# Optimization experiments

Hardware: AMD Instinct MI355X
Metric: run time of the kernel (lower is better)

## Reference

```python
import jax, jax.numpy as jnp
import numpy as np

N_NODES = 60000
N_EDGES = 240000
N_REL = 4
N_GRAPHS = 128
D_IN = 768
D_H = 256
N_LAYERS = 6


def setup_inputs() -> dict:
    key = jax.random.key(0)
    ks = jax.random.split(key, 16)
    x = jax.random.normal(ks[0], (N_NODES, D_IN), dtype=jnp.float32)
    edge_index = jax.random.randint(ks[1], (2, N_EDGES), 0, N_NODES, dtype=jnp.int64)
    edge_attr = jax.random.randint(ks[2], (N_EDGES,), 0, N_REL, dtype=jnp.int64)
    batch = jnp.sort(jax.random.randint(ks[3], (N_NODES,), 0, N_GRAPHS, dtype=jnp.int64))
    s0 = 1.0 / np.sqrt(D_IN)
    s1 = 1.0 / np.sqrt(D_H)
    w0 = jax.random.normal(ks[4], (N_REL, D_IN, D_H), dtype=jnp.float32) * s0
    root0 = jax.random.normal(ks[5], (D_IN, D_H), dtype=jnp.float32) * s0
    b0 = jnp.zeros((D_H,), jnp.float32)
    w_rest = jax.random.normal(ks[6], (N_LAYERS - 1, N_REL, D_H, D_H), dtype=jnp.float32) * s1
    root_rest = jax.random.normal(ks[7], (N_LAYERS - 1, D_H, D_H), dtype=jnp.float32) * s1
    b_rest = jnp.zeros((N_LAYERS - 1, D_H), jnp.float32)
    fc1_w = jax.random.normal(ks[8], (2 * D_H, 128), dtype=jnp.float32) * (1.0 / np.sqrt(2 * D_H))
    fc1_b = jnp.zeros((128,), jnp.float32)
    fc2_w = jax.random.normal(ks[9], (128, 1), dtype=jnp.float32) * (1.0 / np.sqrt(128))
    fc2_b = jnp.zeros((1,), jnp.float32)
    return {"x": x, "edge_index": edge_index, "edge_attr": edge_attr, "batch": batch,
            "w0": w0, "root0": root0, "b0": b0,
            "w_rest": w_rest, "root_rest": root_rest, "b_rest": b_rest,
            "fc1_w": fc1_w, "fc1_b": fc1_b, "fc2_w": fc2_w, "fc2_b": fc2_b}


def _rgcn(h, src, dst, rel, W, root, b):
    # PyG RGCNConv with aggr='mean': per-relation mean over incoming edges,
    # transformed by per-relation weight, plus root transform and bias.
    n = h.shape[0]
    seg = rel * n + dst                                   # combined (relation, target) segment id
    msgs = h[src]                                         # [E, d_in] gather
    agg = jax.ops.segment_sum(msgs, seg, num_segments=N_REL * n)
    agg = agg.reshape(N_REL, n, -1)                       # [R, N, d_in]
    cnt = jax.ops.segment_sum(jnp.ones_like(rel, jnp.float32), seg, num_segments=N_REL * n)
    cnt = cnt.reshape(N_REL, n, 1)
    mean = agg / jnp.maximum(cnt, 1.0)                    # mean aggregation; 0 for isolated nodes
    return jnp.einsum('rnd,rdo->no', mean, W) + h @ root + b


def reference(x, edge_index, edge_attr, batch, w0, root0, b0,
              w_rest, root_rest, b_rest, fc1_w, fc1_b, fc2_w, fc2_b):
    src, dst = edge_index[0], edge_index[1]
    h = jax.nn.relu(_rgcn(x, src, dst, edge_attr, w0, root0, b0))
    for i in range(N_LAYERS - 1):
        h = jax.nn.relu(_rgcn(h, src, dst, edge_attr, w_rest[i], root_rest[i], b_rest[i]))
    # global mean / max pooling over graphs
    sums = jax.ops.segment_sum(h, batch, num_segments=N_GRAPHS)
    cnt = jax.ops.segment_sum(jnp.ones((h.shape[0],), jnp.float32), batch, num_segments=N_GRAPHS)[:, None]
    h_mean = sums / jnp.maximum(cnt, 1.0)
    h_max = jax.ops.segment_max(h, batch, num_segments=N_GRAPHS)
    h_max = jnp.where(cnt > 0, h_max, 0.0)
    g = jnp.concatenate([h_mean, h_max], axis=1)          # [G, 512]
    out = jax.nn.relu(g @ fc1_w + fc1_b)                  # dropout is identity at inference
    out = out @ fc2_w + fc2_b
    return jax.nn.sigmoid(out.squeeze(-1))                # [G]
```

## Files before the change

kernel.cpp:

```cpp
#include <hip/hip_runtime.h>
#include <hip/hip_bf16.h>

#define N_NODES  60000
#define N_EDGES  240000
#define N_REL    4
#define N_GRAPHS 128
#define D_IN     768
#define D_H      256
#define N_LAYERS 6
#define M_PAD    60032
#define N_TOT    1280
#define BM_L     64
#define LDM      264

static inline int cdiv(int a, int b) { return (a + b - 1) / b; }

typedef __attribute__((ext_vector_type(8))) short short8;
typedef __attribute__((ext_vector_type(4))) float f32x4;

__device__ __forceinline__ float bf2f(unsigned short u) {
    union { unsigned int i; float f; } c; c.i = ((unsigned int)u) << 16; return c.f;
}
__device__ __forceinline__ float bflo(unsigned int u) {
    union { unsigned int i; float f; } c; c.i = u << 16; return c.f;
}
__device__ __forceinline__ float bfhi(unsigned int u) {
    union { unsigned int i; float f; } c; c.i = u & 0xffff0000u; return c.f;
}
__device__ __forceinline__ unsigned short f2bf(float f) {
    union { float f; unsigned int i; } c; c.f = f;
    unsigned int i = c.i;
    unsigned int r = (i + 0x7FFFu + ((i >> 16) & 1u)) >> 16;
    return (unsigned short)r;
}

__device__ __forceinline__ void gload16(const void* g, void* l) {
    __builtin_amdgcn_global_load_lds((const __attribute__((address_space(1))) void*)g,
                                     (__attribute__((address_space(3))) void*)l, 16, 0, 0);
}

__device__ __forceinline__ void accum32(float4* am, uint4 v0, uint4 v1, uint4 v2, uint4 v3) {
    am[0].x += bflo(v0.x); am[0].y += bfhi(v0.x);
    am[0].z += bflo(v0.y); am[0].w += bfhi(v0.y);
    am[1].x += bflo(v0.z); am[1].y += bfhi(v0.z);
    am[1].z += bflo(v0.w); am[1].w += bfhi(v0.w);
    am[2].x += bflo(v1.x); am[2].y += bfhi(v1.x);
    am[2].z += bflo(v1.y); am[2].w += bfhi(v1.y);
    am[3].x += bflo(v1.z); am[3].y += bfhi(v1.z);
    am[3].z += bflo(v1.w); am[3].w += bfhi(v1.w);
    am[4].x += bflo(v2.x); am[4].y += bfhi(v2.x);
    am[4].z += bflo(v2.y); am[4].w += bfhi(v2.y);
    am[5].x += bflo(v2.z); am[5].y += bfhi(v2.z);
    am[5].z += bflo(v2.w); am[5].w += bfhi(v2.w);
    am[6].x += bflo(v3.x); am[6].y += bfhi(v3.x);
    am[6].z += bflo(v3.y); am[6].w += bfhi(v3.y);
    am[7].x += bflo(v3.z); am[7].y += bfhi(v3.z);
    am[7].z += bflo(v3.w); am[7].w += bfhi(v3.w);
}

__global__ __launch_bounds__(512) void gemm_l0(
    const unsigned short* __restrict__ A,
    const unsigned short* __restrict__ Bt,
    const float* __restrict__ bias,
    unsigned short* __restrict__ out_root,
    unsigned short* __restrict__ out_msg,
    int K)
{
    __shared__ unsigned short As[128 * 32];
    __shared__ unsigned short Bs[256 * 32];

    const int tid  = threadIdx.x;
    const int wave = tid >> 6, lane = tid & 63;

    int b = blockIdx.x;
    int bm, bn;
    if (b < 2320) { int grp = b / 40, rem = b % 40; bm = (grp * 8 + (rem & 7)) * 128; bn = (rem >> 3) * 256; }
    else          { int rem = b - 2320; bm = (464 + rem % 5) * 128; bn = (rem / 5) * 256; }

    const int wm = (wave & 1) * 64, wn = (wave >> 1) * 64;

    const int lr = lane >> 2;
    const int kg = ((lane & 3) ^ ((lr ^ (lr >> 2)) & 3)) * 8;
    const unsigned short* gsrc[3];
    unsigned short* ldst[3];
    #pragma unroll
    for (int j = 0; j < 3; ++j) {
        int g = wave * 3 + j;
        if (g < 8) {
            gsrc[j] = A + (size_t)(bm + g * 16 + lr) * K + kg;
            ldst[j] = As + g * 16 * 32;
        } else {
            gsrc[j] = Bt + (size_t)(bn + (g - 8) * 16 + lr) * K + kg;
            ldst[j] = Bs + (g - 8) * 16 * 32;
        }
    }

    f32x4 acc[4][4] = {};
    const int fr = lane & 15;
    const int qsw = (((lane >> 4) ^ fr ^ (fr >> 2)) & 3) * 8;

    for (int k0 = 0; k0 < K; k0 += 32) {
        gload16(gsrc[0] + k0, ldst[0]);
        gload16(gsrc[1] + k0, ldst[1]);
        gload16(gsrc[2] + k0, ldst[2]);
        __syncthreads();

        short8 a[4], bb[4];
        #pragma unroll
        for (int t = 0; t < 4; ++t) {
            a[t]  = *(const short8*)&As[(wm + t * 16 + fr) * 32 + qsw];
            bb[t] = *(const short8*)&Bs[(wn + t * 16 + fr) * 32 + qsw];
        }
        #pragma unroll
        for (int mt = 0; mt < 4; ++mt)
            #pragma unroll
            for (int nt = 0; nt < 4; ++nt)
                acc[mt][nt] = __builtin_amdgcn_mfma_f32_16x16x32_bf16(
                    a[mt], bb[nt], acc[mt][nt], 0, 0, 0);
        __syncthreads();
    }

    const bool is_root = (bn == 0);
    #pragma unroll
    for (int mt = 0; mt < 4; ++mt) {
        #pragma unroll
        for (int nt = 0; nt < 4; ++nt) {
            int col = bn + wn + nt * 16 + fr;
            float bv = bias[col];
            #pragma unroll
            for (int r = 0; r < 4; ++r) {
                int row = bm + wm + mt * 16 + ((lane >> 4) << 2) + r;
                float v = acc[mt][nt][r] + bv;
                if (is_root) out_root[(size_t)row * 256 + col] = f2bf(v);
                else         out_msg[(size_t)row * 1024 + (col - 256)] = f2bf(v);
            }
        }
    }
}

__global__ __launch_bounds__(512) void rgcn_layer(
    const unsigned short* __restrict__ h,
    const unsigned short* __restrict__ Wl,
    const float* __restrict__ bias,
    const int* __restrict__ rp4,
    const int* __restrict__ e_srcs,
    const float* __restrict__ inv4,
    unsigned short* __restrict__ h_out)
{
    __shared__ unsigned short mt[BM_L * LDM];

    const int tid  = threadIdx.x;
    const int wave = tid >> 6, lane = tid & 63;
    const int bm = blockIdx.x * BM_L;

    const int node  = bm + lane;
    const int cq    = wave * 32;
    const bool valid = node < N_NODES;

    const int fr   = lane & 15;
    const int q8   = (lane >> 4) * 8;
    const int wcol = wave * 32;

    const unsigned short* w0p = Wl + (size_t)(wcol + fr) * N_TOT + q8;
    const unsigned short* w1p = Wl + (size_t)(wcol + 16 + fr) * N_TOT + q8;

    float4 iv = valid ? *(const float4*)&inv4[(size_t)node * 4]
                      : make_float4(1.f, 1.f, 1.f, 1.f);

    f32x4 acc[4][2] = {};

    for (int r = 0; r < 5; ++r) {
        float4 am[8];
        #pragma unroll
        for (int j = 0; j < 8; ++j) am[j] = make_float4(0.f, 0.f, 0.f, 0.f);

        if (r < 4) {
            if (valid) {
                int lo = rp4[(size_t)node * 4 + r];
                int hi = rp4[(size_t)node * 4 + r + 1];
                int e = lo;
                for (; e + 1 < hi; e += 2) {
                    const uint4* p0 = (const uint4*)(h + (size_t)e_srcs[e] * 256 + cq);
                    const uint4* p1 = (const uint4*)(h + (size_t)e_srcs[e + 1] * 256 + cq);
                    uint4 v0 = p0[0], v1 = p0[1], v2 = p0[2], v3 = p0[3];
                    uint4 u0 = p1[0], u1 = p1[1], u2 = p1[2], u3 = p1[3];
                    accum32(am, v0, v1, v2, v3);
                    accum32(am, u0, u1, u2, u3);
                }
                if (e < hi) {
                    const uint4* p0 = (const uint4*)(h + (size_t)e_srcs[e] * 256 + cq);
                    accum32(am, p0[0], p0[1], p0[2], p0[3]);
                }
            }
        } else {
            const uint4* p0 = (const uint4*)(h + (size_t)node * 256 + cq);
            accum32(am, p0[0], p0[1], p0[2], p0[3]);
        }
        float sc = (r == 0) ? iv.x : (r == 1) ? iv.y : (r == 2) ? iv.z
                 : (r == 3) ? iv.w : 1.f;

        __syncthreads();
        {
            unsigned short* dst = &mt[lane * LDM + cq];
            #pragma unroll
            for (int j = 0; j < 8; ++j) {
                ushort4 o;
                o.x = f2bf(am[j].x * sc); o.y = f2bf(am[j].y * sc);
                o.z = f2bf(am[j].z * sc); o.w = f2bf(am[j].w * sc);
                *(ushort4*)(dst + j * 4) = o;
            }
        }
        __syncthreads();

        const int rOff = (r << 8);
        #pragma unroll
        for (int kk = 0; kk < 8; ++kk) {
            short8 b0 = *(const short8*)(w0p + rOff + kk * 32);
            short8 b1 = *(const short8*)(w1p + rOff + kk * 32);
            short8 a[4];
            #pragma unroll
            for (int i = 0; i < 4; ++i)
                a[i] = *(const short8*)&mt[(i * 16 + fr) * LDM + kk * 32 + q8];
            #pragma unroll
            for (int i = 0; i < 4; ++i) {
                acc[i][0] = __builtin_amdgcn_mfma_f32_16x16x32_bf16(a[i], b0, acc[i][0], 0, 0, 0);
                acc[i][1] = __builtin_amdgcn_mfma_f32_16x16x32_bf16(a[i], b1, acc[i][1], 0, 0, 0);
            }
        }
    }

    #pragma unroll
    for (int i = 0; i < 4; ++i) {
        #pragma unroll
        for (int nt = 0; nt < 2; ++nt) {
            int col = wcol + nt * 16 + fr;
            float bv = bias[col];
            #pragma unroll
            for (int rg = 0; rg < 4; ++rg) {
                int row = bm + i * 16 + ((lane >> 4) << 2) + rg;
                float v = fmaxf(acc[i][nt][rg] + bv, 0.f);
                h_out[(size_t)row * 256 + col] = f2bf(v);
            }
        }
    }
}

__global__ void convert_x(const float* __restrict__ x, unsigned short* __restrict__ xb) {
    size_t i = ((size_t)blockIdx.x * 256 + threadIdx.x) * 4;
    if (i >= (size_t)M_PAD * D_IN) return;
    ushort4 o;
    if (i < (size_t)N_NODES * D_IN) {
        float4 v = *(const float4*)&x[i];
        o.x = f2bf(v.x); o.y = f2bf(v.y); o.z = f2bf(v.z); o.w = f2bf(v.w);
    } else {
        o.x = o.y = o.z = o.w = 0;
    }
    *(ushort4*)&xb[i] = o;
}

__global__ void pack_w0(const float* __restrict__ root0, const float* __restrict__ w0,
                        unsigned short* __restrict__ Wt0) {
    int idx = blockIdx.x * 256 + threadIdx.x;
    if (idx >= N_TOT * D_IN) return;
    int k = idx % D_IN, n = idx / D_IN;
    float v = (n < 256) ? root0[k * 256 + n]
                        : w0[(((n >> 8) - 1) * D_IN + k) * 256 + (n & 255)];
    Wt0[idx] = f2bf(v);
}

__global__ void pack_wr(const float* __restrict__ root_rest, const float* __restrict__ w_rest,
                        unsigned short* __restrict__ WtR) {
    int idx = blockIdx.x * 256 + threadIdx.x;
    if (idx >= 5 * 256 * N_TOT) return;
    int k = idx % N_TOT; int t = idx / N_TOT; int n = t & 255; int l = t >> 8;
    float v = (k < 1024)
        ? w_rest[(((l * 4 + (k >> 8)) * 256) + (k & 255)) * 256 + n]
        : root_rest[(l * 256 + (k - 1024)) * 256 + n];
    WtR[idx] = f2bf(v);
}

__global__ void build_bias(const float* __restrict__ b0, float* __restrict__ eb) {
    int i = blockIdx.x * 256 + threadIdx.x;
    if (i < N_TOT) eb[i] = (i < 256) ? b0[i] : 0.f;
}

__global__ void deg4_count(const int* __restrict__ dst, const int* __restrict__ rel,
                           int* __restrict__ deg4, int E) {
    int e = blockIdx.x * 256 + threadIdx.x;
    if (e < E) atomicAdd(&deg4[dst[e] * 4 + rel[e]], 1);
}

__global__ void invert4(const int* __restrict__ deg4, float* __restrict__ inv4, int n) {
    int i = blockIdx.x * 256 + threadIdx.x;
    if (i < n) inv4[i] = 1.0f / (float)max(deg4[i], 1);
}

__global__ __launch_bounds__(256) void block_sum(const int* __restrict__ deg,
                                                 int* __restrict__ bsum, int n) {
    __shared__ int s[256];
    int i = blockIdx.x * 256 + threadIdx.x;
    s[threadIdx.x] = (i < n) ? deg[i] : 0;
    __syncthreads();
    for (int o = 128; o > 0; o >>= 1) {
        if (threadIdx.x < o) s[threadIdx.x] += s[threadIdx.x + o];
        __syncthreads();
    }
    if (threadIdx.x == 0) bsum[blockIdx.x] = s[0];
}

__global__ __launch_bounds__(1024) void scan_bsum(const int* __restrict__ bsum,
                                                  int* __restrict__ boff, int nb) {
    __shared__ int s[1024];
    int t = threadIdx.x;
    int v0 = (t < nb) ? bsum[t] : 0;
    s[t] = v0;
    __syncthreads();
    for (int o = 1; o < 1024; o <<= 1) {
        int v = (t >= o) ? s[t - o] : 0;
        __syncthreads();
        s[t] += v;
        __syncthreads();
    }
    if (t < nb) boff[t] = s[t] - v0;
}

__global__ __launch_bounds__(256) void block_scan_write(
    const int* __restrict__ deg, const int* __restrict__ boff,
    int* __restrict__ row_ptr, int* __restrict__ cursor, int n, int total) {
    __shared__ int s[256];
    int t = threadIdx.x;
    int i = blockIdx.x * 256 + t;
    int v = (i < n) ? deg[i] : 0;
    s[t] = v;
    __syncthreads();
    for (int o = 1; o < 256; o <<= 1) {
        int u = (t >= o) ? s[t - o] : 0;
        __syncthreads();
        s[t] += u;
        __syncthreads();
    }
    int excl = s[t] - v + boff[blockIdx.x];
    if (i < n) { row_ptr[i] = excl; cursor[i] = excl; }
    if (blockIdx.x == 0 && t == 0) row_ptr[n] = total;
}

__global__ void place_edges4(const int* __restrict__ dst, const int* __restrict__ src,
                             const int* __restrict__ rel, int* __restrict__ cursor,
                             int* __restrict__ e_srcs, int E) {
    int e = blockIdx.x * 256 + threadIdx.x;
    if (e < E) {
        int p = atomicAdd(&cursor[dst[e] * 4 + rel[e]], 1);
        e_srcs[p] = src[e];
    }
}

__global__ __launch_bounds__(256) void aggregate0(
    const unsigned short* __restrict__ rootb,
    const unsigned short* __restrict__ msg,
    const int* __restrict__ rp4, const int* __restrict__ e_srcs,
    const float* __restrict__ inv4,
    unsigned short* __restrict__ h_out)
{
    int node = blockIdx.x * 4 + (threadIdx.x >> 6);
    if (node >= N_NODES) return;
    int lane = threadIdx.x & 63;
    float4 iv = *(const float4*)&inv4[(size_t)node * 4];

    ushort4 rt = *(const ushort4*)&rootb[(size_t)node * 256 + lane * 4];
    float4 acc = make_float4(bf2f(rt.x), bf2f(rt.y), bf2f(rt.z), bf2f(rt.w));

    #pragma unroll
    for (int r = 0; r < 4; ++r) {
        int lo = rp4[(size_t)node * 4 + r], hi = rp4[(size_t)node * 4 + r + 1];
        float f = (r == 0) ? iv.x : (r == 1) ? iv.y : (r == 2) ? iv.z : iv.w;
        float4 s4 = make_float4(0, 0, 0, 0);
        int e = lo;
        for (; e + 1 < hi; e += 2) {
            ushort4 m0 = *(const ushort4*)&msg[(size_t)e_srcs[e] * 1024 + (r << 8) + lane * 4];
            ushort4 m1 = *(const ushort4*)&msg[(size_t)e_srcs[e + 1] * 1024 + (r << 8) + lane * 4];
            s4.x += bf2f(m0.x) + bf2f(m1.x);
            s4.y += bf2f(m0.y) + bf2f(m1.y);
            s4.z += bf2f(m0.z) + bf2f(m1.z);
            s4.w += bf2f(m0.w) + bf2f(m1.w);
        }
        if (e < hi) {
            ushort4 m0 = *(const ushort4*)&msg[(size_t)e_srcs[e] * 1024 + (r << 8) + lane * 4];
            s4.x += bf2f(m0.x); s4.y += bf2f(m0.y);
            s4.z += bf2f(m0.z); s4.w += bf2f(m0.w);
        }
        acc.x += s4.x * f; acc.y += s4.y * f;
        acc.z += s4.z * f; acc.w += s4.w * f;
    }
    ushort4 o;
    o.x = f2bf(fmaxf(acc.x, 0.f));
    o.y = f2bf(fmaxf(acc.y, 0.f));
    o.z = f2bf(fmaxf(acc.z, 0.f));
    o.w = f2bf(fmaxf(acc.w, 0.f));
    *(ushort4*)&h_out[(size_t)node * 256 + lane * 4] = o;
}

__global__ __launch_bounds__(256) void pool_kernel(
    const unsigned short* __restrict__ h, const int* __restrict__ batch,
    float* __restrict__ g_feat)
{
    int g = blockIdx.x;
    int t = threadIdx.x;
    __shared__ int s_lo, s_hi;
    if (t == 0) {
        int lo = 0, hi = N_NODES;
        while (lo < hi) { int m = (lo + hi) >> 1; if (batch[m] < g) lo = m + 1; else hi = m; }
        s_lo = lo;
        int lo2 = lo, hi2 = N_NODES;
        while (lo2 < hi2) { int m = (lo2 + hi2) >> 1; if (batch[m] < g + 1) lo2 = m + 1; else hi2 = m; }
        s_hi = lo2;
    }
    __syncthreads();
    int lo = s_lo, hi = s_hi;
    float sum = 0.f, mx = 0.f;
    for (int n = lo; n < hi; ++n) {
        float v = bf2f(h[(size_t)n * 256 + t]);
        sum += v;
        mx = fmaxf(mx, v);
    }
    float cnt = (float)(hi - lo);
    g_feat[g * 512 + t]       = sum / fmaxf(cnt, 1.0f);
    g_feat[g * 512 + 256 + t] = (cnt > 0.f) ? mx : 0.f;
}

__global__ __launch_bounds__(128) void mlp_head(
    const float* __restrict__ g_feat,
    const float* __restrict__ fc1_w, const float* __restrict__ fc1_b,
    const float* __restrict__ fc2_w, const float* __restrict__ fc2_b,
    float* __restrict__ out)
{
    __shared__ float gf[512];
    __shared__ float partial[2];
    int g = blockIdx.x, t = threadIdx.x;
    for (int i = t; i < 512; i += 128) gf[i] = g_feat[g * 512 + i];
    __syncthreads();
    float acc = fc1_b[t];
    for (int i = 0; i < 512; ++i) acc += gf[i] * fc1_w[i * 128 + t];
    float h1 = fmaxf(acc, 0.f);
    float v = h1 * fc2_w[t];
    #pragma unroll
    for (int off = 32; off > 0; off >>= 1) v += __shfl_down(v, off);
    if ((t & 63) == 0) partial[t >> 6] = v;
    __syncthreads();
    if (t == 0) {
        float s = partial[0] + partial[1] + fc2_b[0];
        out[g] = 1.0f / (1.0f + expf(-s));
    }
}

extern "C" void kernel_launch(void* const* d_in, const int* in_sizes, int n_in,
                              void* d_out, int out_size, void* d_ws, size_t ws_size,
                              hipStream_t stream) {
    const float* x          = (const float*)d_in[0];
    const int*   edge_index = (const int*)d_in[1];
    const int*   edge_attr  = (const int*)d_in[2];
    const int*   batch      = (const int*)d_in[3];
    const float* w0         = (const float*)d_in[4];
    const float* root0      = (const float*)d_in[5];
    const float* b0         = (const float*)d_in[6];
    const float* w_rest     = (const float*)d_in[7];
    const float* root_rest  = (const float*)d_in[8];
    const float* b_rest     = (const float*)d_in[9];
    const float* fc1_w      = (const float*)d_in[10];
    const float* fc1_b      = (const float*)d_in[11];
    const float* fc2_w      = (const float*)d_in[12];
    const float* fc2_b      = (const float*)d_in[13];
    float* out = (float*)d_out;

    const int* e_src = edge_index;
    const int* e_dst = edge_index + N_EDGES;

    char* p = (char*)d_ws;
    auto alloc = [&](size_t bytes) { char* q = p; p += (bytes + 255) & ~(size_t)255; return q; };
    unsigned short* x_bf   = (unsigned short*)alloc((size_t)M_PAD * D_IN * 2);
    unsigned short* msgbuf = (unsigned short*)alloc((size_t)M_PAD * 1024 * 2);
    unsigned short* hA     = (unsigned short*)alloc((size_t)M_PAD * 256 * 2);
    unsigned short* hB     = (unsigned short*)alloc((size_t)M_PAD * 256 * 2);
    unsigned short* Wt0    = (unsigned short*)alloc((size_t)N_TOT * D_IN * 2);
    unsigned short* WtR    = (unsigned short*)alloc((size_t)5 * 256 * N_TOT * 2);
    float*          ebias  = (float*)alloc(N_TOT * 4);
    float*          inv4   = (float*)alloc((size_t)N_NODES * 4 * 4);
    float*          g_feat = (float*)alloc((size_t)N_GRAPHS * 512 * 4);
    int*            deg4   = (int*)alloc((size_t)N_NODES * 4 * 4);
    int*            rp4    = (int*)alloc(((size_t)N_NODES * 4 + 1) * 4);
    int*            cursor4= (int*)alloc((size_t)N_NODES * 4 * 4);
    int*            bsum   = (int*)alloc(1024 * 4);
    int*            boff   = (int*)alloc(1024 * 4);
    int*            e_srcs = (int*)alloc((size_t)N_EDGES * 4);

    const int n4 = N_NODES * 4;
    const int nscan4 = cdiv(n4, 256);

    hipMemsetAsync(deg4, 0, (size_t)n4 * 4, stream);
    convert_x<<<cdiv(M_PAD * D_IN / 4, 256), 256, 0, stream>>>(x, x_bf);
    pack_w0<<<cdiv(N_TOT * D_IN, 256), 256, 0, stream>>>(root0, w0, Wt0);
    pack_wr<<<cdiv(5 * 256 * N_TOT, 256), 256, 0, stream>>>(root_rest, w_rest, WtR);
    build_bias<<<cdiv(N_TOT, 256), 256, 0, stream>>>(b0, ebias);
    deg4_count<<<cdiv(N_EDGES, 256), 256, 0, stream>>>(e_dst, edge_attr, deg4, N_EDGES);
    invert4<<<cdiv(n4, 256), 256, 0, stream>>>(deg4, inv4, n4);
    block_sum<<<nscan4, 256, 0, stream>>>(deg4, bsum, n4);
    scan_bsum<<<1, 1024, 0, stream>>>(bsum, boff, nscan4);
    block_scan_write<<<nscan4, 256, 0, stream>>>(deg4, boff, rp4, cursor4, n4, N_EDGES);
    place_edges4<<<cdiv(N_EDGES, 256), 256, 0, stream>>>(e_dst, e_src, edge_attr,
                                                         cursor4, e_srcs, N_EDGES);

    gemm_l0<<<2345, 512, 0, stream>>>(x_bf, Wt0, ebias, hB, msgbuf, D_IN);
    aggregate0<<<cdiv(N_NODES, 4), 256, 0, stream>>>(hB, msgbuf, rp4, e_srcs, inv4, hA);

    unsigned short* cur = hA;
    unsigned short* nxt = hB;
    for (int L = 1; L < N_LAYERS; ++L) {
        rgcn_layer<<<M_PAD / BM_L, 512, 0, stream>>>(
            cur, WtR + (size_t)(L - 1) * 256 * N_TOT, b_rest + (size_t)(L - 1) * 256,
            rp4, e_srcs, inv4, nxt);
        unsigned short* t = cur; cur = nxt; nxt = t;
    }

    pool_kernel<<<N_GRAPHS, 256, 0, stream>>>(cur, batch, g_feat);
    mlp_head<<<N_GRAPHS, 128, 0, stream>>>(g_feat, fc1_w, fc1_b, fc2_w, fc2_b, out);
}
```

Baseline: 1.368 ms.

## Stage layer weights through swizzled LDS and fold prep kernels into scan

The per-layer RGCN kernel now copies each 32-wide K slice of the weight matrix into a swizzled shared-memory tile with async 16-byte loads, instead of having every wave read B fragments straight from global memory. This adds barriers per K step and disables unrolling of that loop. Separately, the bias build and degree inversion are folded into other prep kernels to cut launches. The edge placement now also precomputes per-edge message offsets and mean weights, so aggregate0 runs one flat weighted loop over all relations.

```diff
diff --git a/kernel.cpp b/kernel.cpp
--- a/kernel.cpp
+++ b/kernel.cpp
@@ -148,6 +148,7 @@
     unsigned short* __restrict__ h_out)
 {
     __shared__ unsigned short mt[BM_L * LDM];
+    __shared__ unsigned short Bs[256 * 32];
 
     const int tid  = threadIdx.x;
     const int wave = tid >> 6, lane = tid & 63;
@@ -157,12 +158,13 @@
     const int cq    = wave * 32;
     const bool valid = node < N_NODES;
 
+    const int lr = lane >> 2;
+    const int kg = ((lane & 3) ^ ((lr ^ (lr >> 2)) & 3)) * 8;
+
     const int fr   = lane & 15;
     const int q8   = (lane >> 4) * 8;
+    const int qsw = (((lane >> 4) ^ fr ^ (fr >> 2)) & 3) * 8;
     const int wcol = wave * 32;
-
-    const unsigned short* w0p = Wl + (size_t)(wcol + fr) * N_TOT + q8;
-    const unsigned short* w1p = Wl + (size_t)(wcol + 16 + fr) * N_TOT + q8;
 
     float4 iv = valid ? *(const float4*)&inv4[(size_t)node * 4]
                       : make_float4(1.f, 1.f, 1.f, 1.f);
@@ -170,6 +172,16 @@
     f32x4 acc[4][2] = {};
 
     for (int r = 0; r < 5; ++r) {
+        const int rOff = r << 8;
+
+        __syncthreads();
+
+        {
+            int g0 = wave * 2;
+            gload16(Wl + (size_t)(g0 * 16 + lr) * N_TOT + rOff + kg, Bs + g0 * 512);
+            gload16(Wl + (size_t)((g0 + 1) * 16 + lr) * N_TOT + rOff + kg, Bs + (g0 + 1) * 512);
+        }
+
         float4 am[8];
         #pragma unroll
         for (int j = 0; j < 8; ++j) am[j] = make_float4(0.f, 0.f, 0.f, 0.f);
@@ -199,7 +211,6 @@
         float sc = (r == 0) ? iv.x : (r == 1) ? iv.y : (r == 2) ? iv.z
                  : (r == 3) ? iv.w : 1.f;
 
-        __syncthreads();
         {
             unsigned short* dst = &mt[lane * LDM + cq];
             #pragma unroll
@@ -210,21 +221,29 @@
                 *(ushort4*)(dst + j * 4) = o;
             }
         }
-        __syncthreads();
-
-        const int rOff = (r << 8);
-        #pragma unroll
+
+        #pragma unroll 1
         for (int kk = 0; kk < 8; ++kk) {
-            short8 b0 = *(const short8*)(w0p + rOff + kk * 32);
-            short8 b1 = *(const short8*)(w1p + rOff + kk * 32);
-            short8 a[4];
+            if (kk > 0) {
+                __syncthreads();
+                int g0 = wave * 2;
+                gload16(Wl + (size_t)(g0 * 16 + lr) * N_TOT + rOff + kg + kk * 32,
+                        Bs + g0 * 512);
+                gload16(Wl + (size_t)((g0 + 1) * 16 + lr) * N_TOT + rOff + kg + kk * 32,
+                        Bs + (g0 + 1) * 512);
+            }
+            __syncthreads();
+
+            short8 a4[4], b0, b1;
             #pragma unroll
             for (int i = 0; i < 4; ++i)
-                a[i] = *(const short8*)&mt[(i * 16 + fr) * LDM + kk * 32 + q8];
+                a4[i] = *(const short8*)&mt[(i * 16 + fr) * LDM + kk * 32 + q8];
+            b0 = *(const short8*)&Bs[(wcol + fr) * 32 + qsw];
+            b1 = *(const short8*)&Bs[(wcol + 16 + fr) * 32 + qsw];
             #pragma unroll
             for (int i = 0; i < 4; ++i) {
-                acc[i][0] = __builtin_amdgcn_mfma_f32_16x16x32_bf16(a[i], b0, acc[i][0], 0, 0, 0);
-                acc[i][1] = __builtin_amdgcn_mfma_f32_16x16x32_bf16(a[i], b1, acc[i][1], 0, 0, 0);
+                acc[i][0] = __builtin_amdgcn_mfma_f32_16x16x32_bf16(a4[i], b0, acc[i][0], 0, 0, 0);
+                acc[i][1] = __builtin_amdgcn_mfma_f32_16x16x32_bf16(a4[i], b1, acc[i][1], 0, 0, 0);
             }
         }
     }
@@ -259,8 +278,10 @@
 }
 
 __global__ void pack_w0(const float* __restrict__ root0, const float* __restrict__ w0,
+                        const float* __restrict__ b0, float* __restrict__ eb,
                         unsigned short* __restrict__ Wt0) {
     int idx = blockIdx.x * 256 + threadIdx.x;
+    if (idx < N_TOT) eb[idx] = (idx < 256) ? b0[idx] : 0.f;
     if (idx >= N_TOT * D_IN) return;
     int k = idx % D_IN, n = idx / D_IN;
     float v = (n < 256) ? root0[k * 256 + n]
@@ -279,20 +300,10 @@
     WtR[idx] = f2bf(v);
 }
 
-__global__ void build_bias(const float* __restrict__ b0, float* __restrict__ eb) {
-    int i = blockIdx.x * 256 + threadIdx.x;
-    if (i < N_TOT) eb[i] = (i < 256) ? b0[i] : 0.f;
-}
-
 __global__ void deg4_count(const int* __restrict__ dst, const int* __restrict__ rel,
                            int* __restrict__ deg4, int E) {
     int e = blockIdx.x * 256 + threadIdx.x;
     if (e < E) atomicAdd(&deg4[dst[e] * 4 + rel[e]], 1);
-}
-
-__global__ void invert4(const int* __restrict__ deg4, float* __restrict__ inv4, int n) {
-    int i = blockIdx.x * 256 + threadIdx.x;
-    if (i < n) inv4[i] = 1.0f / (float)max(deg4[i], 1);
 }
 
 __global__ __launch_bounds__(256) void block_sum(const int* __restrict__ deg,
@@ -326,7 +337,8 @@
 
 __global__ __launch_bounds__(256) void block_scan_write(
     const int* __restrict__ deg, const int* __restrict__ boff,
-    int* __restrict__ row_ptr, int* __restrict__ cursor, int n, int total) {
+    int* __restrict__ row_ptr, int* __restrict__ cursor,
+    float* __restrict__ inv4, int n, int total) {
     __shared__ int s[256];
     int t = threadIdx.x;
     int i = blockIdx.x * 256 + t;
@@ -340,63 +352,72 @@
         __syncthreads();
     }
     int excl = s[t] - v + boff[blockIdx.x];
-    if (i < n) { row_ptr[i] = excl; cursor[i] = excl; }
+    if (i < n) {
+        row_ptr[i] = excl; cursor[i] = excl;
+        inv4[i] = 1.0f / (float)max(v, 1);
+    }
     if (blockIdx.x == 0 && t == 0) row_ptr[n] = total;
 }
 
 __global__ void place_edges4(const int* __restrict__ dst, const int* __restrict__ src,
-                             const int* __restrict__ rel, int* __restrict__ cursor,
-                             int* __restrict__ e_srcs, int E) {
+                             const int* __restrict__ rel, const float* __restrict__ inv4,
+                             int* __restrict__ cursor,
+                             int* __restrict__ e_srcs, int* __restrict__ eoff,
+                             float* __restrict__ ew, int E) {
     int e = blockIdx.x * 256 + threadIdx.x;
     if (e < E) {
-        int p = atomicAdd(&cursor[dst[e] * 4 + rel[e]], 1);
-        e_srcs[p] = src[e];
+        int d = dst[e], r = rel[e], s = src[e];
+        int seg = d * 4 + r;
+        int p = atomicAdd(&cursor[seg], 1);
+        e_srcs[p] = s;
+        eoff[p]   = s * 4 + r;
+        ew[p]     = inv4[seg];
     }
 }
 
 __global__ __launch_bounds__(256) void aggregate0(
     const unsigned short* __restrict__ rootb,
     const unsigned short* __restrict__ msg,
-    const int* __restrict__ rp4, const int* __restrict__ e_srcs,
-    const float* __restrict__ inv4,
+    const int* __restrict__ rp4, const int* __restrict__ eoff,
+    const float* __restrict__ ew,
     unsigned short* __restrict__ h_out)
 {
     int node = blockIdx.x * 4 + (threadIdx.x >> 6);
     if (node >= N_NODES) return;
     int lane = threadIdx.x & 63;
-    float4 iv = *(const float4*)&inv4[(size_t)node * 4];
-
-    ushort4 rt = *(const ushort4*)&rootb[(size_t)node * 256 + lane * 4];
+    const int cc = lane * 4;
+
+    ushort4 rt = *(const ushort4*)&rootb[(size_t)node * 256 + cc];
     float4 acc = make_float4(bf2f(rt.x), bf2f(rt.y), bf2f(rt.z), bf2f(rt.w));
 
-    #pragma unroll
-    for (int r = 0; r < 4; ++r) {
-        int lo = rp4[(size_t)node * 4 + r], hi = rp4[(size_t)node * 4 + r + 1];
-        float f = (r == 0) ? iv.x : (r == 1) ? iv.y : (r == 2) ? iv.z : iv.w;
-        float4 s4 = make_float4(0, 0, 0, 0);
-        int e = lo;
-        for (; e + 1 < hi; e += 2) {
-            ushort4 m0 = *(const ushort4*)&msg[(size_t)e_srcs[e] * 1024 + (r << 8) + lane * 4];
-            ushort4 m1 = *(const ushort4*)&msg[(size_t)e_srcs[e + 1] * 1024 + (r << 8) + lane * 4];
-            s4.x += bf2f(m0.x) + bf2f(m1.x);
-            s4.y += bf2f(m0.y) + bf2f(m1.y);
-            s4.z += bf2f(m0.z) + bf2f(m1.z);
-            s4.w += bf2f(m0.w) + bf2f(m1.w);
-        }
-        if (e < hi) {
-            ushort4 m0 = *(const ushort4*)&msg[(size_t)e_srcs[e] * 1024 + (r << 8) + lane * 4];
-            s4.x += bf2f(m0.x); s4.y += bf2f(m0.y);
-            s4.z += bf2f(m0.z); s4.w += bf2f(m0.w);
-        }
-        acc.x += s4.x * f; acc.y += s4.y * f;
-        acc.z += s4.z * f; acc.w += s4.w * f;
+    int lo = rp4[(size_t)node * 4];
+    int hi = rp4[(size_t)node * 4 + 4];
+    int e = lo;
+    for (; e + 3 < hi; e += 4) {
+        int o0 = eoff[e], o1 = eoff[e + 1], o2 = eoff[e + 2], o3 = eoff[e + 3];
+        float w0 = ew[e], w1 = ew[e + 1], w2 = ew[e + 2], w3 = ew[e + 3];
+        ushort4 m0 = *(const ushort4*)&msg[(size_t)o0 * 256 + cc];
+        ushort4 m1 = *(const ushort4*)&msg[(size_t)o1 * 256 + cc];
+        ushort4 m2 = *(const ushort4*)&msg[(size_t)o2 * 256 + cc];
+        ushort4 m3 = *(const ushort4*)&msg[(size_t)o3 * 256 + cc];
+        acc.x += w0 * bf2f(m0.x) + w1 * bf2f(m1.x) + w2 * bf2f(m2.x) + w3 * bf2f(m3.x);
+        acc.y += w0 * bf2f(m0.y) + w1 * bf2f(m1.y) + w2 * bf2f(m2.y) + w3 * bf2f(m3.y);
+        acc.z += w0 * bf2f(m0.z) + w1 * bf2f(m1.z) + w2 * bf2f(m2.z) + w3 * bf2f(m3.z);
+        acc.w += w0 * bf2f(m0.w) + w1 * bf2f(m1.w) + w2 * bf2f(m2.w) + w3 * bf2f(m3.w);
+    }
+    for (; e < hi; ++e) {
+        int o0 = eoff[e];
+        float w0 = ew[e];
+        ushort4 m0 = *(const ushort4*)&msg[(size_t)o0 * 256 + cc];
+        acc.x += w0 * bf2f(m0.x); acc.y += w0 * bf2f(m0.y);
+        acc.z += w0 * bf2f(m0.z); acc.w += w0 * bf2f(m0.w);
     }
     ushort4 o;
     o.x = f2bf(fmaxf(acc.x, 0.f));
     o.y = f2bf(fmaxf(acc.y, 0.f));
     o.z = f2bf(fmaxf(acc.z, 0.f));
     o.w = f2bf(fmaxf(acc.w, 0.f));
-    *(ushort4*)&h_out[(size_t)node * 256 + lane * 4] = o;
+    *(ushort4*)&h_out[(size_t)node * 256 + cc] = o;
 }
 
 __global__ __launch_bounds__(256) void pool_kernel(
@@ -491,25 +512,25 @@
     int*            bsum   = (int*)alloc(1024 * 4);
     int*            boff   = (int*)alloc(1024 * 4);
     int*            e_srcs = (int*)alloc((size_t)N_EDGES * 4);
+    int*            eoff   = (int*)alloc((size_t)N_EDGES * 4);
+    float*          ew     = (float*)alloc((size_t)N_EDGES * 4);
 
     const int n4 = N_NODES * 4;
     const int nscan4 = cdiv(n4, 256);
 
     hipMemsetAsync(deg4, 0, (size_t)n4 * 4, stream);
     convert_x<<<cdiv(M_PAD * D_IN / 4, 256), 256, 0, stream>>>(x, x_bf);
-    pack_w0<<<cdiv(N_TOT * D_IN, 256), 256, 0, stream>>>(root0, w0, Wt0);
+    pack_w0<<<cdiv(N_TOT * D_IN, 256), 256, 0, stream>>>(root0, w0, b0, ebias, Wt0);
     pack_wr<<<cdiv(5 * 256 * N_TOT, 256), 256, 0, stream>>>(root_rest, w_rest, WtR);
-    build_bias<<<cdiv(N_TOT, 256), 256, 0, stream>>>(b0, ebias);
     deg4_count<<<cdiv(N_EDGES, 256), 256, 0, stream>>>(e_dst, edge_attr, deg4, N_EDGES);
-    invert4<<<cdiv(n4, 256), 256, 0, stream>>>(deg4, inv4, n4);
     block_sum<<<nscan4, 256, 0, stream>>>(deg4, bsum, n4);
     scan_bsum<<<1, 1024, 0, stream>>>(bsum, boff, nscan4);
-    block_scan_write<<<nscan4, 256, 0, stream>>>(deg4, boff, rp4, cursor4, n4, N_EDGES);
-    place_edges4<<<cdiv(N_EDGES, 256), 256, 0, stream>>>(e_dst, e_src, edge_attr,
-                                                         cursor4, e_srcs, N_EDGES);
+    block_scan_write<<<nscan4, 256, 0, stream>>>(deg4, boff, rp4, cursor4, inv4, n4, N_EDGES);
+    place_edges4<<<cdiv(N_EDGES, 256), 256, 0, stream>>>(e_dst, e_src, edge_attr, inv4,
+                                                         cursor4, e_srcs, eoff, ew, N_EDGES);
 
     gemm_l0<<<2345, 512, 0, stream>>>(x_bf, Wt0, ebias, hB, msgbuf, D_IN);
-    aggregate0<<<cdiv(N_NODES, 4), 256, 0, stream>>>(hB, msgbuf, rp4, e_srcs, inv4, hA);
+    aggregate0<<<cdiv(N_NODES, 4), 256, 0, stream>>>(hB, msgbuf, rp4, eoff, ew, hA);
 
     unsigned short* cur = hA;
     unsigned short* nxt = hB;
```

Measured after the change: 1.474 ms. 1.08x slower.

## Stage weight tiles in LDS, transpose weight packing via shared memory, simplify gather loop

Applied to the files above, without the earlier changes.

The rgcn_layer kernel now loads each 256x32 weight k-slice into a swizzled LDS buffer once per block (via gload16) instead of every wave reading its B fragments directly from global memory. This adds a barrier per k-step in exchange for shared reuse of the weight tile. The weight packing kernels are replaced with tiled 32x32 shared-memory transposes so both global reads and writes are coalesced. The aggregate0 edge loop is also simplified from a 2-way unrolled loop to a plain single-edge loop.

```diff
diff --git a/kernel.cpp b/kernel.cpp
--- a/kernel.cpp
+++ b/kernel.cpp
@@ -148,6 +148,7 @@
     unsigned short* __restrict__ h_out)
 {
     __shared__ unsigned short mt[BM_L * LDM];
+    __shared__ unsigned short Bs[256 * 32];
 
     const int tid  = threadIdx.x;
     const int wave = tid >> 6, lane = tid & 63;
@@ -157,12 +158,13 @@
     const int cq    = wave * 32;
     const bool valid = node < N_NODES;
 
-    const int fr   = lane & 15;
-    const int q8   = (lane >> 4) * 8;
+    const int lr = lane >> 2;
+    const int kg = ((lane & 3) ^ ((lr ^ (lr >> 2)) & 3)) * 8;
+
+    const int fr  = lane & 15;
+    const int q8  = (lane >> 4) * 8;
+    const int qsw = (((lane >> 4) ^ fr ^ (fr >> 2)) & 3) * 8;
     const int wcol = wave * 32;
-
-    const unsigned short* w0p = Wl + (size_t)(wcol + fr) * N_TOT + q8;
-    const unsigned short* w1p = Wl + (size_t)(wcol + 16 + fr) * N_TOT + q8;
 
     float4 iv = valid ? *(const float4*)&inv4[(size_t)node * 4]
                       : make_float4(1.f, 1.f, 1.f, 1.f);
@@ -210,23 +212,33 @@
                 *(ushort4*)(dst + j * 4) = o;
             }
         }
-        __syncthreads();
-
-        const int rOff = (r << 8);
-        #pragma unroll
+
+        const int rOff = r << 8;
+        #pragma unroll 1
         for (int kk = 0; kk < 8; ++kk) {
-            short8 b0 = *(const short8*)(w0p + rOff + kk * 32);
-            short8 b1 = *(const short8*)(w1p + rOff + kk * 32);
-            short8 a[4];
+            if (kk > 0) __syncthreads();
+            {
+                int g0 = wave * 2;
+                gload16(Wl + (size_t)(g0 * 16 + lr) * N_TOT + rOff + kg + kk * 32,
+                        Bs + g0 * 512);
+                gload16(Wl + (size_t)((g0 + 1) * 16 + lr) * N_TOT + rOff + kg + kk * 32,
+                        Bs + (g0 + 1) * 512);
+            }
+            __syncthreads();
+
+            short8 a4[4], b0, b1;
             #pragma unroll
             for (int i = 0; i < 4; ++i)
-                a[i] = *(const short8*)&mt[(i * 16 + fr) * LDM + kk * 32 + q8];
+                a4[i] = *(const short8*)&mt[(i * 16 + fr) * LDM + kk * 32 + q8];
+            b0 = *(const short8*)&Bs[(wcol + fr) * 32 + qsw];
+            b1 = *(const short8*)&Bs[(wcol + 16 + fr) * 32 + qsw];
             #pragma unroll
             for (int i = 0; i < 4; ++i) {
-                acc[i][0] = __builtin_amdgcn_mfma_f32_16x16x32_bf16(a[i], b0, acc[i][0], 0, 0, 0);
-                acc[i][1] = __builtin_amdgcn_mfma_f32_16x16x32_bf16(a[i], b1, acc[i][1], 0, 0, 0);
+                acc[i][0] = __builtin_amdgcn_mfma_f32_16x16x32_bf16(a4[i], b0, acc[i][0], 0, 0, 0);
+                acc[i][1] = __builtin_amdgcn_mfma_f32_16x16x32_bf16(a4[i], b1, acc[i][1], 0, 0, 0);
             }
         }
+        __syncthreads();
     }
 
     #pragma unroll
@@ -258,25 +270,49 @@
     *(ushort4*)&xb[i] = o;
 }
 
-__global__ void pack_w0(const float* __restrict__ root0, const float* __restrict__ w0,
-                        unsigned short* __restrict__ Wt0) {
-    int idx = blockIdx.x * 256 + threadIdx.x;
-    if (idx >= N_TOT * D_IN) return;
-    int k = idx % D_IN, n = idx / D_IN;
-    float v = (n < 256) ? root0[k * 256 + n]
-                        : w0[(((n >> 8) - 1) * D_IN + k) * 256 + (n & 255)];
-    Wt0[idx] = f2bf(v);
-}
-
-__global__ void pack_wr(const float* __restrict__ root_rest, const float* __restrict__ w_rest,
-                        unsigned short* __restrict__ WtR) {
-    int idx = blockIdx.x * 256 + threadIdx.x;
-    if (idx >= 5 * 256 * N_TOT) return;
-    int k = idx % N_TOT; int t = idx / N_TOT; int n = t & 255; int l = t >> 8;
-    float v = (k < 1024)
-        ? w_rest[(((l * 4 + (k >> 8)) * 256) + (k & 255)) * 256 + n]
-        : root_rest[(l * 256 + (k - 1024)) * 256 + n];
-    WtR[idx] = f2bf(v);
+__global__ __launch_bounds__(256) void pack_w0_t(
+    const float* __restrict__ root0, const float* __restrict__ w0,
+    unsigned short* __restrict__ Wt0)
+{
+    __shared__ float t[32][33];
+    int b = blockIdx.x;
+    int i  = b / 192;
+    int rem = b % 192;
+    int kb = (rem / 8) * 32;
+    int nb = (rem % 8) * 32;
+    const float* S = (i == 0) ? root0 : w0 + (size_t)(i - 1) * D_IN * 256;
+    int tx = threadIdx.x & 31, ty = threadIdx.x >> 5;
+    #pragma unroll
+    for (int j = 0; j < 4; ++j)
+        t[ty + j * 8][tx] = S[(size_t)(kb + ty + j * 8) * 256 + nb + tx];
+    __syncthreads();
+    #pragma unroll
+    for (int j = 0; j < 4; ++j)
+        Wt0[(size_t)(i * 256 + nb + ty + j * 8) * D_IN + kb + tx] = f2bf(t[tx][ty + j * 8]);
+}
+
+__global__ __launch_bounds__(256) void pack_wr_t(
+    const float* __restrict__ root_rest, const float* __restrict__ w_rest,
+    unsigned short* __restrict__ WtR)
+{
+    __shared__ float t[32][33];
+    int b = blockIdx.x;
+    int m = b / 64;
+    int rem = b % 64;
+    int kb = (rem / 8) * 32;
+    int nb = (rem % 8) * 32;
+    int l = m / 5, j = m % 5;
+    const float* S = (j < 4) ? w_rest + (size_t)(l * 4 + j) * 256 * 256
+                             : root_rest + (size_t)l * 256 * 256;
+    int tx = threadIdx.x & 31, ty = threadIdx.x >> 5;
+    #pragma unroll
+    for (int jj = 0; jj < 4; ++jj)
+        t[ty + jj * 8][tx] = S[(size_t)(kb + ty + jj * 8) * 256 + nb + tx];
+    __syncthreads();
+    #pragma unroll
+    for (int jj = 0; jj < 4; ++jj)
+        WtR[(size_t)(l * 256 + nb + ty + jj * 8) * N_TOT + j * 256 + kb + tx] =
+            f2bf(t[tx][ty + jj * 8]);
 }
 
 __global__ void build_bias(const float* __restrict__ b0, float* __restrict__ eb) {
@@ -374,19 +410,11 @@
         int lo = rp4[(size_t)node * 4 + r], hi = rp4[(size_t)node * 4 + r + 1];
         float f = (r == 0) ? iv.x : (r == 1) ? iv.y : (r == 2) ? iv.z : iv.w;
         float4 s4 = make_float4(0, 0, 0, 0);
-        int e = lo;
-        for (; e + 1 < hi; e += 2) {
-            ushort4 m0 = *(const ushort4*)&msg[(size_t)e_srcs[e] * 1024 + (r << 8) + lane * 4];
-            ushort4 m1 = *(const ushort4*)&msg[(size_t)e_srcs[e + 1] * 1024 + (r << 8) + lane * 4];
-            s4.x += bf2f(m0.x) + bf2f(m1.x);
-            s4.y += bf2f(m0.y) + bf2f(m1.y);
-            s4.z += bf2f(m0.z) + bf2f(m1.z);
-            s4.w += bf2f(m0.w) + bf2f(m1.w);
-        }
-        if (e < hi) {
-            ushort4 m0 = *(const ushort4*)&msg[(size_t)e_srcs[e] * 1024 + (r << 8) + lane * 4];
-            s4.x += bf2f(m0.x); s4.y += bf2f(m0.y);
-            s4.z += bf2f(m0.z); s4.w += bf2f(m0.w);
+        for (int e = lo; e < hi; ++e) {
+            int s = e_srcs[e];
+            ushort4 m = *(const ushort4*)&msg[(size_t)s * 1024 + (r << 8) + lane * 4];
+            s4.x += bf2f(m.x); s4.y += bf2f(m.y);
+            s4.z += bf2f(m.z); s4.w += bf2f(m.w);
         }
         acc.x += s4.x * f; acc.y += s4.y * f;
         acc.z += s4.z * f; acc.w += s4.w * f;
@@ -497,8 +525,8 @@
 
     hipMemsetAsync(deg4, 0, (size_t)n4 * 4, stream);
     convert_x<<<cdiv(M_PAD * D_IN / 4, 256), 256, 0, stream>>>(x, x_bf);
-    pack_w0<<<cdiv(N_TOT * D_IN, 256), 256, 0, stream>>>(root0, w0, Wt0);
-    pack_wr<<<cdiv(5 * 256 * N_TOT, 256), 256, 0, stream>>>(root_rest, w_rest, WtR);
+    pack_w0_t<<<960, 256, 0, stream>>>(root0, w0, Wt0);
+    pack_wr_t<<<1600, 256, 0, stream>>>(root_rest, w_rest, WtR);
     build_bias<<<cdiv(N_TOT, 256), 256, 0, stream>>>(b0, ebias);
     deg4_count<<<cdiv(N_EDGES, 256), 256, 0, stream>>>(e_dst, edge_attr, deg4, N_EDGES);
     invert4<<<cdiv(n4, 256), 256, 0, stream>>>(deg4, inv4, n4);
```

Measured after the change: 1.468 ms. 1.07x slower.
